# Kernel tuning notes

Measured on AMD Instinct MI355X. Metric: run time of the kernel, lower is better.

## Reference

```python
import jax, jax.numpy as jnp
import numpy as np

B, T, H = 32, 2048, 1024

def setup_inputs() -> dict:
    key = jax.random.key(0)
    ks = jax.random.split(key, 8)
    s = 1.0 / np.sqrt(H)
    return {
        "query": jax.random.normal(ks[0], (B, H), dtype=jnp.float32),
        "values": jax.random.normal(ks[1], (B, T, H), dtype=jnp.float32),
        "Wq": jax.random.uniform(ks[2], (H, H), jnp.float32, -s, s),
        "bq": jax.random.uniform(ks[3], (H,), jnp.float32, -s, s),
        "Wv": jax.random.uniform(ks[4], (H, H), jnp.float32, -s, s),
        "bv": jax.random.uniform(ks[5], (H,), jnp.float32, -s, s),
        "Vw": jax.random.uniform(ks[6], (1, H), jnp.float32, -s, s),
        "Vb": jax.random.uniform(ks[7], (1,), jnp.float32, -s, s),
    }

def reference(query, values, Wq, bq, Wv, bv, Vw, Vb):
    # q_proj: [B,1,H], v_proj: [B,T,H]
    q_proj = (query @ Wq.T + bq)[:, None, :]
    v_proj = jnp.einsum('bth,oh->bto', values, Wv) + bv
    # score: [B,T,1] = tanh(...) @ Vw.T + Vb
    score = jnp.einsum('bth,oh->bto', jnp.tanh(q_proj + v_proj), Vw) + Vb
    attention_weights = jax.nn.softmax(score, axis=1)  # over time
    context_vector = jnp.sum(attention_weights * values, axis=1)  # [B,H]
    return (context_vector, attention_weights)
```

## Files before the change

### kernel.cpp

```cpp
#include <hip/hip_runtime.h>

#define BATCH 32
#define TT    2048
#define HH    1024
#define MTOT  (BATCH * TT)

typedef unsigned short ushort_t;
typedef short sh8 __attribute__((ext_vector_type(8)));
typedef float f4 __attribute__((ext_vector_type(4)));
typedef unsigned short us8 __attribute__((ext_vector_type(8)));

__device__ __forceinline__ ushort_t f2bf(float f) {
    unsigned u = __float_as_uint(f);
    u = (u + 0x7fffu + ((u >> 16) & 1u)) >> 16;
    return (ushort_t)u;
}
__device__ __forceinline__ float bf2f(ushort_t h) {
    return __uint_as_float(((unsigned)h) << 16);
}
__device__ __forceinline__ float fast_tanh(float x) {
    float e = __expf(2.0f * x);
    return 1.0f - 2.0f * __builtin_amdgcn_rcpf(e + 1.0f);
}

__device__ __forceinline__ void glds16(const void* g, void* l) {
    __builtin_amdgcn_global_load_lds(
        (const __attribute__((address_space(1))) void*)g,
        (__attribute__((address_space(3))) void*)l, 16, 0, 0);
}

__global__ void cvt_bf16_k(const float* __restrict__ in, ushort_t* __restrict__ out, long n) {
    long i = ((long)blockIdx.x * blockDim.x + threadIdx.x) * 8;
    if (i + 8 > n) return;
    float4 a = *(const float4*)(in + i);
    float4 b = *(const float4*)(in + i + 4);
    us8 o;
    o[0]=f2bf(a.x); o[1]=f2bf(a.y); o[2]=f2bf(a.z); o[3]=f2bf(a.w);
    o[4]=f2bf(b.x); o[5]=f2bf(b.y); o[6]=f2bf(b.z); o[7]=f2bf(b.w);
    *(us8*)(out + i) = o;
}

__global__ void qproj_k(const float* __restrict__ query, const float* __restrict__ Wq,
                        const float* __restrict__ bq, const float* __restrict__ bv,
                        float* __restrict__ qp) {
    int o = blockIdx.x, tid = threadIdx.x;
    float4 w4 = *(const float4*)(Wq + (long)o * HH + tid * 4);
    __shared__ float sm[BATCH][4];
    int wid = tid >> 6, lane = tid & 63;
    for (int b = 0; b < BATCH; ++b) {
        float4 q4 = *(const float4*)(query + (long)b * HH + tid * 4);
        float p = q4.x*w4.x + q4.y*w4.y + q4.z*w4.z + q4.w*w4.w;
        #pragma unroll
        for (int m = 1; m < 64; m <<= 1) p += __shfl_xor(p, m);
        if (lane == 0) sm[b][wid] = p;
    }
    __syncthreads();
    if (tid < BATCH) {
        float s = sm[tid][0] + sm[tid][1] + sm[tid][2] + sm[tid][3] + bq[o] + bv[o];
        qp[(long)tid * HH + o] = s;
    }
}

#define BM 128
#define BN 128
#define BK 64

__global__ __launch_bounds__(256, 2) void score_gemm_k(
    const ushort_t* __restrict__ A, const ushort_t* __restrict__ Bw,
    const float* __restrict__ qp, const float* __restrict__ Vw,
    float* __restrict__ score)
{
    __shared__ ushort_t As[BM * BK];
    __shared__ ushort_t Bs[BN * BK];
    int tid = threadIdx.x;

    int bx = blockIdx.x;
    int x  = bx & 7;
    int s  = bx >> 3;
    int nt = s & 7;
    int mt = ((s >> 3) << 3) | x;
    const long m0 = (long)mt * BM;
    const int  n0 = nt * BN;

    int wid  = tid >> 6, lane = tid & 63;
    int quad = lane >> 4, l16 = lane & 15;
    int wrow = (wid >> 1) * 64, wcol = (wid & 1) * 64;

    f4 acc[4][4] = {};

    int srow = tid >> 3;
    int sseg = tid & 7;
    int xseg = sseg ^ (srow & 7);
    const ushort_t* Ag = A  + (m0 + srow) * (long)HH + xseg * 8;
    const ushort_t* Bg = Bw + (long)(n0 + srow) * HH + xseg * 8;
    char* AsB = (char*)As;
    char* BsB = (char*)Bs;
    const int ldsOff = wid * 1024;

    for (int kt = 0; kt < HH / BK; ++kt) {
        const int kb = kt * BK;
        #pragma unroll
        for (int c = 0; c < 4; ++c) {
            glds16(Ag + (long)c * 32 * HH + kb, AsB + c * 4096 + ldsOff);
            glds16(Bg + (long)c * 32 * HH + kb, BsB + c * 4096 + ldsOff);
        }
        __syncthreads();

        sh8 af[4][2], bf[4][2];
        #pragma unroll
        for (int i = 0; i < 4; ++i) {
            int r = wrow + i * 16 + l16;
            #pragma unroll
            for (int kq = 0; kq < 2; ++kq) {
                int sg = (kq * 4 + quad) ^ (r & 7);
                af[i][kq] = *(const sh8*)(AsB + r * 128 + sg * 16);
            }
        }
        #pragma unroll
        for (int j = 0; j < 4; ++j) {
            int r = wcol + j * 16 + l16;
            #pragma unroll
            for (int kq = 0; kq < 2; ++kq) {
                int sg = (kq * 4 + quad) ^ (r & 7);
                bf[j][kq] = *(const sh8*)(BsB + r * 128 + sg * 16);
            }
        }
        #pragma unroll
        for (int kq = 0; kq < 2; ++kq)
            #pragma unroll
            for (int i = 0; i < 4; ++i)
                #pragma unroll
                for (int j = 0; j < 4; ++j)
                    acc[i][j] = __builtin_amdgcn_mfma_f32_16x16x32_bf16(
                        af[i][kq], bf[j][kq], acc[i][j], 0, 0, 0);
        __syncthreads();
    }

    int bidx = (int)(m0 >> 11);
    const float* qpb = qp + (long)bidx * HH;
    float qv[4], vw[4];
    #pragma unroll
    for (int j = 0; j < 4; ++j) {
        int cg = n0 + wcol + j * 16 + l16;
        qv[j] = qpb[cg];
        vw[j] = Vw[cg];
    }
    #pragma unroll
    for (int i = 0; i < 4; ++i) {
        #pragma unroll
        for (int r = 0; r < 4; ++r) {
            float sum = 0.0f;
            #pragma unroll
            for (int j = 0; j < 4; ++j) {
                float xv = acc[i][j][r] + qv[j];
                sum += fast_tanh(xv) * vw[j];
            }
            sum += __shfl_xor(sum, 1);
            sum += __shfl_xor(sum, 2);
            sum += __shfl_xor(sum, 4);
            sum += __shfl_xor(sum, 8);
            if (l16 == 0) {
                atomicAdd(score + m0 + wrow + i * 16 + quad * 4 + r, sum);
            }
        }
    }
}

__global__ void softmax_k(const float* __restrict__ sc, float* __restrict__ w) {
    int b = blockIdx.x, tid = threadIdx.x;
    const float* s = sc + (long)b * TT;
    float v[8];
    float4 a0 = *(const float4*)(s + tid * 8);
    float4 a1 = *(const float4*)(s + tid * 8 + 4);
    v[0]=a0.x; v[1]=a0.y; v[2]=a0.z; v[3]=a0.w;
    v[4]=a1.x; v[5]=a1.y; v[6]=a1.z; v[7]=a1.w;
    float mx = v[0];
    #pragma unroll
    for (int i = 1; i < 8; ++i) mx = fmaxf(mx, v[i]);
    #pragma unroll
    for (int m = 1; m < 64; m <<= 1) mx = fmaxf(mx, __shfl_xor(mx, m));
    __shared__ float smx[4], ssum[4];
    int wid = tid >> 6;
    if ((tid & 63) == 0) smx[wid] = mx;
    __syncthreads();
    mx = fmaxf(fmaxf(smx[0], smx[1]), fmaxf(smx[2], smx[3]));
    float sum = 0.0f;
    #pragma unroll
    for (int i = 0; i < 8; ++i) { v[i] = __expf(v[i] - mx); sum += v[i]; }
    #pragma unroll
    for (int m = 1; m < 64; m <<= 1) sum += __shfl_xor(sum, m);
    if ((tid & 63) == 0) ssum[wid] = sum;
    __syncthreads();
    sum = ssum[0] + ssum[1] + ssum[2] + ssum[3];
    float inv = 1.0f / sum;
    float4 o0 = make_float4(v[0]*inv, v[1]*inv, v[2]*inv, v[3]*inv);
    float4 o1 = make_float4(v[4]*inv, v[5]*inv, v[6]*inv, v[7]*inv);
    *(float4*)(w + (long)b * TT + tid * 8)     = o0;
    *(float4*)(w + (long)b * TT + tid * 8 + 4) = o1;
}

__global__ void context_k2(const ushort_t* __restrict__ vb, const float* __restrict__ w,
                           float* __restrict__ partial) {
    int b = blockIdx.x, tc = blockIdx.y;
    int tid = threadIdx.x;
    int toff = tid >> 7;
    int hi   = tid & 127;
    int h    = hi * 8;
    __shared__ float sw[128];
    __shared__ float red[128][8];
    if (tid < 128) sw[tid] = w[(long)b * TT + tc * 128 + tid];
    __syncthreads();

    const ushort_t* base = vb + ((long)b * TT + tc * 128 + toff) * HH + h;
    float acc[8] = {0.f,0.f,0.f,0.f,0.f,0.f,0.f,0.f};
    #pragma unroll 8
    for (int it = 0; it < 64; ++it) {
        us8 v = *(const us8*)(base + (long)it * 2 * HH);
        float wt = sw[it * 2 + toff];
        #pragma unroll
        for (int e = 0; e < 8; ++e) acc[e] += wt * bf2f(v[e]);
    }
    if (toff == 1) {
        #pragma unroll
        for (int e = 0; e < 8; ++e) red[hi][e] = acc[e];
    }
    __syncthreads();
    if (toff == 0) {
        #pragma unroll
        for (int e = 0; e < 8; ++e) acc[e] += red[hi][e];
        float* p = partial + ((long)tc * 32 + b) * HH + h;
        *(float4*)(p)     = make_float4(acc[0], acc[1], acc[2], acc[3]);
        *(float4*)(p + 4) = make_float4(acc[4], acc[5], acc[6], acc[7]);
    }
}

__global__ void context_red_k(const float* __restrict__ partial, float* __restrict__ ctx) {
    int i = blockIdx.x * 256 + threadIdx.x;
    float s = 0.f;
    #pragma unroll
    for (int tc = 0; tc < 16; ++tc) s += partial[(long)tc * 32768 + i];
    ctx[i] = s;
}

extern "C" void kernel_launch(void* const* d_in, const int* in_sizes, int n_in,
                              void* d_out, int out_size, void* d_ws, size_t ws_size,
                              hipStream_t stream) {
    const float* query  = (const float*)d_in[0];
    const float* values = (const float*)d_in[1];
    const float* Wq     = (const float*)d_in[2];
    const float* bq     = (const float*)d_in[3];
    const float* Wv     = (const float*)d_in[4];
    const float* bv     = (const float*)d_in[5];
    const float* Vw     = (const float*)d_in[6];

    char* ws = (char*)d_ws;
    ushort_t* vb   = (ushort_t*)ws;
    ushort_t* wvb  = (ushort_t*)(ws + 134217728);
    float*    qp   = (float*)   (ws + 134217728 + 2097152);
    float*    scre = (float*)   (ws + 134217728 + 2097152 + 131072);
    float*    partial = (float*)wvb;

    float* ctx  = (float*)d_out;
    float* wout = (float*)d_out + BATCH * HH;

    hipMemsetAsync(scre, 0, (size_t)MTOT * 4, stream);

    cvt_bf16_k<<<(BATCH * TT * HH) / 2048, 256, 0, stream>>>(values, vb, (long)BATCH * TT * HH);
    cvt_bf16_k<<<(HH * HH) / 2048, 256, 0, stream>>>(Wv, wvb, (long)HH * HH);

    qproj_k<<<HH, 256, 0, stream>>>(query, Wq, bq, bv, qp);

    score_gemm_k<<<(MTOT / BM) * (HH / BN), 256, 0, stream>>>(vb, wvb, qp, Vw, scre);

    softmax_k<<<BATCH, 256, 0, stream>>>(scre, wout);

    context_k2<<<dim3(BATCH, 16), 256, 0, stream>>>(vb, wout, partial);
    context_red_k<<<(BATCH * HH) / 256, 256, 0, stream>>>(partial, ctx);
}
```

Before: 565.3 us.

## Fuse fp32-to-bf16 conversion of values into score GEMM and read fp32 in context

```diff
diff --git a/kernel.cpp b/kernel.cpp
--- a/kernel.cpp
+++ b/kernel.cpp
@@ -15,8 +15,11 @@
     u = (u + 0x7fffu + ((u >> 16) & 1u)) >> 16;
     return (ushort_t)u;
 }
-__device__ __forceinline__ float bf2f(ushort_t h) {
-    return __uint_as_float(((unsigned)h) << 16);
+__device__ __forceinline__ unsigned pack2(float x, float y) {
+    unsigned a = __float_as_uint(x), b = __float_as_uint(y);
+    a = a + 0x7fffu + ((a >> 16) & 1u);
+    b = b + 0x7fffu + ((b >> 16) & 1u);
+    return (a >> 16) | (b & 0xffff0000u);
 }
 __device__ __forceinline__ float fast_tanh(float x) {
     float e = __expf(2.0f * x);
@@ -66,12 +69,12 @@
 #define BK 64
 
 __global__ __launch_bounds__(256, 2) void score_gemm_k(
-    const ushort_t* __restrict__ A, const ushort_t* __restrict__ Bw,
+    const float* __restrict__ A, const ushort_t* __restrict__ Bw,
     const float* __restrict__ qp, const float* __restrict__ Vw,
     float* __restrict__ score)
 {
-    __shared__ ushort_t As[BM * BK];
-    __shared__ ushort_t Bs[BN * BK];
+    __shared__ __align__(16) float    As[BM * BK];
+    __shared__ __align__(16) ushort_t Bs[BN * BK];
     int tid = threadIdx.x;
 
     int bx = blockIdx.x;
@@ -88,32 +91,46 @@
 
     f4 acc[4][4] = {};
 
-    int srow = tid >> 3;
-    int sseg = tid & 7;
-    int xseg = sseg ^ (srow & 7);
-    const ushort_t* Ag = A  + (m0 + srow) * (long)HH + xseg * 8;
-    const ushort_t* Bg = Bw + (long)(n0 + srow) * HH + xseg * 8;
+    int arow  = tid >> 4;
+    int aseg  = tid & 15;
+    int xaseg = aseg ^ arow;
+    const float* Ag = A + (m0 + arow) * (long)HH + xaseg * 4;
+
+    int brow  = tid >> 3;
+    int bseg  = tid & 7;
+    int xbseg = bseg ^ (brow & 7);
+    const ushort_t* Bg = Bw + (long)(n0 + brow) * HH + xbseg * 8;
+
     char* AsB = (char*)As;
     char* BsB = (char*)Bs;
-    const int ldsOff = wid * 1024;
+    const int woff = wid * 1024;
 
     for (int kt = 0; kt < HH / BK; ++kt) {
         const int kb = kt * BK;
         #pragma unroll
-        for (int c = 0; c < 4; ++c) {
-            glds16(Ag + (long)c * 32 * HH + kb, AsB + c * 4096 + ldsOff);
-            glds16(Bg + (long)c * 32 * HH + kb, BsB + c * 4096 + ldsOff);
-        }
+        for (int c = 0; c < 8; ++c)
+            glds16(Ag + (long)c * 16 * HH + kb, AsB + c * 4096 + woff);
+        #pragma unroll
+        for (int c = 0; c < 4; ++c)
+            glds16(Bg + (long)c * 32 * HH + kb, BsB + c * 4096 + woff);
         __syncthreads();
 
         sh8 af[4][2], bf[4][2];
         #pragma unroll
         for (int i = 0; i < 4; ++i) {
             int r = wrow + i * 16 + l16;
+            const char* base = AsB + r * 256;
             #pragma unroll
             for (int kq = 0; kq < 2; ++kq) {
-                int sg = (kq * 4 + quad) ^ (r & 7);
-                af[i][kq] = *(const sh8*)(AsB + r * 128 + sg * 16);
+                int f = kq * 4 + quad;
+                f4 lo = *(const f4*)(base + ((2*f)     ^ l16) * 16);
+                f4 hi = *(const f4*)(base + ((2*f + 1) ^ l16) * 16);
+                int4 p;
+                p.x = pack2(lo[0], lo[1]);
+                p.y = pack2(lo[2], lo[3]);
+                p.z = pack2(hi[0], hi[1]);
+                p.w = pack2(hi[2], hi[3]);
+                af[i][kq] = *(sh8*)&p;
             }
         }
         #pragma unroll
@@ -199,7 +216,7 @@
     *(float4*)(w + (long)b * TT + tid * 8 + 4) = o1;
 }
 
-__global__ void context_k2(const ushort_t* __restrict__ vb, const float* __restrict__ w,
+__global__ void context_k2(const float* __restrict__ values, const float* __restrict__ w,
                            float* __restrict__ partial) {
     int b = blockIdx.x, tc = blockIdx.y;
     int tid = threadIdx.x;
@@ -211,14 +228,15 @@
     if (tid < 128) sw[tid] = w[(long)b * TT + tc * 128 + tid];
     __syncthreads();
 
-    const ushort_t* base = vb + ((long)b * TT + tc * 128 + toff) * HH + h;
+    const float* base = values + ((long)b * TT + tc * 128 + toff) * HH + h;
     float acc[8] = {0.f,0.f,0.f,0.f,0.f,0.f,0.f,0.f};
-    #pragma unroll 8
+    #pragma unroll 4
     for (int it = 0; it < 64; ++it) {
-        us8 v = *(const us8*)(base + (long)it * 2 * HH);
+        float4 v0 = *(const float4*)(base + (long)it * 2 * HH);
+        float4 v1 = *(const float4*)(base + (long)it * 2 * HH + 4);
         float wt = sw[it * 2 + toff];
-        #pragma unroll
-        for (int e = 0; e < 8; ++e) acc[e] += wt * bf2f(v[e]);
+        acc[0] += wt * v0.x; acc[1] += wt * v0.y; acc[2] += wt * v0.z; acc[3] += wt * v0.w;
+        acc[4] += wt * v1.x; acc[5] += wt * v1.y; acc[6] += wt * v1.z; acc[7] += wt * v1.w;
     }
     if (toff == 1) {
         #pragma unroll
@@ -254,26 +272,24 @@
     const float* Vw     = (const float*)d_in[6];
 
     char* ws = (char*)d_ws;
-    ushort_t* vb   = (ushort_t*)ws;
-    ushort_t* wvb  = (ushort_t*)(ws + 134217728);
-    float*    qp   = (float*)   (ws + 134217728 + 2097152);
-    float*    scre = (float*)   (ws + 134217728 + 2097152 + 131072);
-    float*    partial = (float*)wvb;
+    ushort_t* wvb     = (ushort_t*)ws;
+    float*    qp      = (float*)(ws + 2097152);
+    float*    scre    = (float*)(ws + 2097152 + 131072);
+    float*    partial = (float*)(ws + 4194304);
 
     float* ctx  = (float*)d_out;
     float* wout = (float*)d_out + BATCH * HH;
 
     hipMemsetAsync(scre, 0, (size_t)MTOT * 4, stream);
 
-    cvt_bf16_k<<<(BATCH * TT * HH) / 2048, 256, 0, stream>>>(values, vb, (long)BATCH * TT * HH);
     cvt_bf16_k<<<(HH * HH) / 2048, 256, 0, stream>>>(Wv, wvb, (long)HH * HH);
 
     qproj_k<<<HH, 256, 0, stream>>>(query, Wq, bq, bv, qp);
 
-    score_gemm_k<<<(MTOT / BM) * (HH / BN), 256, 0, stream>>>(vb, wvb, qp, Vw, scre);
+    score_gemm_k<<<(MTOT / BM) * (HH / BN), 256, 0, stream>>>(values, wvb, qp, Vw, scre);
 
     softmax_k<<<BATCH, 256, 0, stream>>>(scre, wout);
 
-    context_k2<<<dim3(BATCH, 16), 256, 0, stream>>>(vb, wout, partial);
+    context_k2<<<dim3(BATCH, 16), 256, 0, stream>>>(values, wout, partial);
     context_red_k<<<(BATCH * HH) / 256, 256, 0, stream>>>(partial, ctx);
 }
```

Result: slower. 605.3 us (+7.1%).

## Double-buffer A tile in LDS and load B fragments directly into registers

Applied to the files above, without the earlier changes.

```diff
diff --git a/kernel.cpp b/kernel.cpp
--- a/kernel.cpp
+++ b/kernel.cpp
@@ -70,8 +70,7 @@
     const float* __restrict__ qp, const float* __restrict__ Vw,
     float* __restrict__ score)
 {
-    __shared__ ushort_t As[BM * BK];
-    __shared__ ushort_t Bs[BN * BK];
+    __shared__ ushort_t As[2][BM * BK];
     int tid = threadIdx.x;
 
     int bx = blockIdx.x;
@@ -91,40 +90,59 @@
     int srow = tid >> 3;
     int sseg = tid & 7;
     int xseg = sseg ^ (srow & 7);
-    const ushort_t* Ag = A  + (m0 + srow) * (long)HH + xseg * 8;
-    const ushort_t* Bg = Bw + (long)(n0 + srow) * HH + xseg * 8;
-    char* AsB = (char*)As;
-    char* BsB = (char*)Bs;
-    const int ldsOff = wid * 1024;
+    const ushort_t* Ag = A + (m0 + srow) * (long)HH + xseg * 8;
+    char* AsB0 = (char*)&As[0][0];
+    char* AsB1 = (char*)&As[1][0];
+    const int woff = wid * 1024;
+
+    const ushort_t* Bg[4];
+    #pragma unroll
+    for (int j = 0; j < 4; ++j)
+        Bg[j] = Bw + (long)(n0 + wcol + j * 16 + l16) * HH + quad * 8;
+
+    us8 bcur[4][2], bnext[4][2];
+
+    #pragma unroll
+    for (int c = 0; c < 4; ++c)
+        glds16(Ag + (long)c * 32 * HH, AsB0 + c * 4096 + woff);
+    #pragma unroll
+    for (int j = 0; j < 4; ++j)
+        #pragma unroll
+        for (int kq = 0; kq < 2; ++kq)
+            bcur[j][kq] = *(const us8*)(Bg[j] + kq * 32);
+    __syncthreads();
 
     for (int kt = 0; kt < HH / BK; ++kt) {
         const int kb = kt * BK;
-        #pragma unroll
-        for (int c = 0; c < 4; ++c) {
-            glds16(Ag + (long)c * 32 * HH + kb, AsB + c * 4096 + ldsOff);
-            glds16(Bg + (long)c * 32 * HH + kb, BsB + c * 4096 + ldsOff);
+        char* cb = (kt & 1) ? AsB1 : AsB0;
+        char* nb = (kt & 1) ? AsB0 : AsB1;
+
+        if (kt + 1 < HH / BK) {
+            #pragma unroll
+            for (int c = 0; c < 4; ++c)
+                glds16(Ag + (long)c * 32 * HH + kb + BK, nb + c * 4096 + woff);
         }
-        __syncthreads();
-
-        sh8 af[4][2], bf[4][2];
+
+        sh8 af[4][2];
         #pragma unroll
         for (int i = 0; i < 4; ++i) {
             int r = wrow + i * 16 + l16;
+            const char* base = cb + r * 128;
             #pragma unroll
             for (int kq = 0; kq < 2; ++kq) {
                 int sg = (kq * 4 + quad) ^ (r & 7);
-                af[i][kq] = *(const sh8*)(AsB + r * 128 + sg * 16);
+                af[i][kq] = *(const sh8*)(base + sg * 16);
             }
         }
-        #pragma unroll
-        for (int j = 0; j < 4; ++j) {
-            int r = wcol + j * 16 + l16;
-            #pragma unroll
-            for (int kq = 0; kq < 2; ++kq) {
-                int sg = (kq * 4 + quad) ^ (r & 7);
-                bf[j][kq] = *(const sh8*)(BsB + r * 128 + sg * 16);
-            }
+
+        if (kt + 1 < HH / BK) {
+            #pragma unroll
+            for (int j = 0; j < 4; ++j)
+                #pragma unroll
+                for (int kq = 0; kq < 2; ++kq)
+                    bnext[j][kq] = *(const us8*)(Bg[j] + kb + BK + kq * 32);
         }
+
         #pragma unroll
         for (int kq = 0; kq < 2; ++kq)
             #pragma unroll
@@ -132,7 +150,14 @@
                 #pragma unroll
                 for (int j = 0; j < 4; ++j)
                     acc[i][j] = __builtin_amdgcn_mfma_f32_16x16x32_bf16(
-                        af[i][kq], bf[j][kq], acc[i][j], 0, 0, 0);
+                        af[i][kq], *(sh8*)&bcur[j][kq], acc[i][j], 0, 0, 0);
+
+        #pragma unroll
+        for (int j = 0; j < 4; ++j)
+            #pragma unroll
+            for (int kq = 0; kq < 2; ++kq)
+                bcur[j][kq] = bnext[j][kq];
+
         __syncthreads();
     }
 
```

New measurement: 703.8 us. +24.5%, slower.
